# Kernel optimization log

Hardware: AMD Instinct MI355X
Metric: run time of the kernel (lower is better)

Reference implementation:

```python
import jax, jax.numpy as jnp
import numpy as np

KS = 11
SIGMA = 1.5
DATA_RANGE = 1.0
CHANNELS = 3
C1 = (0.01 * DATA_RANGE) ** 2
C2 = (0.03 * DATA_RANGE) ** 2
EPS = 1e-08


def _gaussian_kernel():
    k1d = jnp.linspace(-(KS // 2), KS // 2, KS, dtype=jnp.float32)
    k1d = jnp.exp(-(k1d ** 2) / (2.0 * SIGMA ** 2))
    k2d = jnp.outer(k1d, k1d)
    k2d = k2d / k2d.sum()
    # depthwise kernel: (out_ch=C, in_ch/groups=1, KH, KW)
    return jnp.tile(k2d[None, None], (CHANNELS, 1, 1, 1))


def setup_inputs() -> dict:
    key = jax.random.key(0)
    k1, k2 = jax.random.split(key)
    B, C, H, W = 32, CHANNELS, 512, 512
    pred = jax.random.normal(k1, (B, C, H, W), dtype=jnp.float32)
    target = jax.random.normal(k2, (B, C, H, W), dtype=jnp.float32)
    kernel = _gaussian_kernel()
    return {"pred": pred, "target": target, "kernel": kernel}


def _dwconv(x, kernel):
    pad = KS // 2
    return jax.lax.conv_general_dilated(
        x, kernel,
        window_strides=(1, 1),
        padding=((pad, pad), (pad, pad)),
        dimension_numbers=("NCHW", "OIHW", "NCHW"),
        feature_group_count=CHANNELS,
    )


def reference(pred, target, kernel):
    # map from [-1,1] to [0, data_range]
    p = (pred + 1.0) / 2.0 * DATA_RANGE
    t = (target + 1.0) / 2.0 * DATA_RANGE

    mu_x = _dwconv(p, kernel)
    mu_y = _dwconv(t, kernel)
    sigma_x = _dwconv(p * p, kernel) - mu_x * mu_x
    sigma_y = _dwconv(t * t, kernel) - mu_y * mu_y
    sigma_xy = _dwconv(p * t, kernel) - mu_x * mu_y

    num = (2.0 * mu_x * mu_y + C1) * (2.0 * sigma_xy + C2)
    den = (mu_x ** 2 + mu_y ** 2 + C1) * (sigma_x + sigma_y + C2)
    ssim_map = num / (den + EPS)
    return jnp.mean(ssim_map, axis=(1, 2, 3))  # per-image SSIM, shape (B,)
```

## Files before the change

kernel.cpp:

```cpp
#include <hip/hip_runtime.h>

typedef float v2f __attribute__((ext_vector_type(2)));
typedef float v4f __attribute__((ext_vector_type(4)));

#define KS     11
#define HWDIM  512
#define IMG    (HWDIM*HWDIM)
#define TH     16
#define STRIPS 32
#define PLANES 96
#define EG2    2
#define QW     132
#define NPARTIAL (PLANES*STRIPS)

__device__ __forceinline__ float ssim_px(float mu_u, float mu_v, float Su, float Sv)
{
    const float C1v = 1e-4f, C2v = 9e-4f, EPSV = 1e-8f;
    const float uu = mu_u*mu_u, vv = mu_v*mu_v;
    const float mu2d = 0.5f*(uu - vv);
    const float mu2s = 0.5f*(uu + vv);
    const float Sd   = 0.5f*(Su - Sv);
    const float Ss   = 0.5f*(Su + Sv);
    const float A  = mu2d + C1v;
    const float B  = Sd - mu2d + C2v;
    const float Cc = mu2s + C1v;
    const float D  = Ss - mu2s + C2v;
    return A * B * __builtin_amdgcn_rcpf(Cc*D + EPSV);
}

#define LOADUV(Y, A, B, C, D) do {                                            \
    if ((unsigned)(Y) < HWDIM) {                                              \
        const v4f p4 = *(const v4f*)(pR + (size_t)(Y)*HWDIM);                 \
        const v4f t4 = *(const v4f*)(tR + (size_t)(Y)*HWDIM);                 \
        A = (v2f){0.5f*(p4.x + t4.x) + 1.0f, 0.5f*(p4.x - t4.x)};             \
        B = (v2f){0.5f*(p4.y + t4.y) + 1.0f, 0.5f*(p4.y - t4.y)};             \
        C = (v2f){0.5f*(p4.z + t4.z) + 1.0f, 0.5f*(p4.z - t4.z)};             \
        D = (v2f){0.5f*(p4.w + t4.w) + 1.0f, 0.5f*(p4.w - t4.w)};             \
    } else { A=(v2f)(0.f); B=(v2f)(0.f); C=(v2f)(0.f); D=(v2f)(0.f); }        \
} while(0)

#define VTAP(W, S) do {                                                       \
    v2f t_;                                                                   \
    t_ = (W)*A##S; mA += t_; SA = __builtin_elementwise_fma(t_, A##S, SA);    \
    t_ = (W)*B##S; mB += t_; SB = __builtin_elementwise_fma(t_, B##S, SB);    \
    t_ = (W)*C##S; mC += t_; SC = __builtin_elementwise_fma(t_, C##S, SC);    \
    t_ = (W)*D##S; mD += t_; SD = __builtin_elementwise_fma(t_, D##S, SD);    \
} while(0)

#define HF(ACC, W, T)                                                         \
    ACC = __builtin_elementwise_fma((v4f){(W),(W),(W),(W)}, (T), ACC)

__global__ __launch_bounds__(128) void ssim_stream_kernel(
    const float* __restrict__ pred,
    const float* __restrict__ target,
    const float* __restrict__ kern,
    float* __restrict__ partial)
{
    __shared__ v4f Pq[2][4][QW];
    __shared__ float red[2];

    const int tid   = threadIdx.x;
    const int strip = blockIdx.x;
    const int plane = blockIdx.y;
    const int y0    = strip * TH;

    const float inv_a5 = 1.0f / sqrtf(kern[60]);
    const float w0  = kern[55]*inv_a5,  w1 = kern[56]*inv_a5;
    const float w2  = kern[57]*inv_a5,  w3 = kern[58]*inv_a5;
    const float w4  = kern[59]*inv_a5,  w5 = kern[60]*inv_a5;
    const float w6  = kern[61]*inv_a5,  w7 = kern[62]*inv_a5;
    const float w8  = kern[63]*inv_a5,  w9 = kern[64]*inv_a5;
    const float w10 = kern[65]*inv_a5;

    const float* pR = pred   + (size_t)plane * IMG + 4*tid;
    const float* tR = target + (size_t)plane * IMG + 4*tid;

    if (tid < EG2) {
        const v4f z = (v4f)(0.f);
        #pragma unroll
        for (int par = 0; par < 2; ++par)
            #pragma unroll
            for (int k = 0; k < 4; ++k) {
                Pq[par][k][tid] = z;
                Pq[par][k][EG2 + 128 + tid] = z;
            }
    }

    v2f A0,A1,A2,A3,A4,A5,A6,A7,A8,A9,A10;
    v2f B0,B1,B2,B3,B4,B5,B6,B7,B8,B9,B10;
    v2f C0,C1,C2,C3,C4,C5,C6,C7,C8,C9,C10;
    v2f D0,D1,D2,D3,D4,D5,D6,D7,D8,D9,D10;
    v2f nA, nB, nC, nD;

    A0=(v2f)(0.f); B0=(v2f)(0.f); C0=(v2f)(0.f); D0=(v2f)(0.f);
    LOADUV(y0-5, A1, B1, C1, D1);
    LOADUV(y0-4, A2, B2, C2, D2);
    LOADUV(y0-3, A3, B3, C3, D3);
    LOADUV(y0-2, A4, B4, C4, D4);
    LOADUV(y0-1, A5, B5, C5, D5);
    LOADUV(y0+0, A6, B6, C6, D6);
    LOADUV(y0+1, A7, B7, C7, D7);
    LOADUV(y0+2, A8, B8, C8, D8);
    LOADUV(y0+3, A9, B9, C9, D9);
    LOADUV(y0+4, A10, B10, C10, D10);
    LOADUV(y0+5, nA, nB, nC, nD);

    float lsum = 0.f;
    for (int r = 0; r < TH; ++r) {
        A0=A1; B0=B1; C0=C1; D0=D1;
        A1=A2; B1=B2; C1=C2; D1=D2;
        A2=A3; B2=B3; C2=C3; D2=D3;
        A3=A4; B3=B4; C3=C4; D3=D4;
        A4=A5; B4=B5; C4=C5; D4=D5;
        A5=A6; B5=B6; C5=C6; D5=D6;
        A6=A7; B6=B7; C6=C7; D6=D7;
        A7=A8; B7=B8; C7=C8; D7=D8;
        A8=A9; B8=B9; C8=C9; D8=D9;
        A9=A10; B9=B10; C9=C10; D9=D10;
        A10=nA; B10=nB; C10=nC; D10=nD;
        LOADUV(y0 + r + 6, nA, nB, nC, nD);

        v2f mA=(v2f)(0.f), SA=(v2f)(0.f), mB=(v2f)(0.f), SB=(v2f)(0.f);
        v2f mC=(v2f)(0.f), SC=(v2f)(0.f), mD=(v2f)(0.f), SD=(v2f)(0.f);
        VTAP(w0,0);  VTAP(w1,1);  VTAP(w2,2);  VTAP(w3,3);  VTAP(w4,4);
        VTAP(w5,5);  VTAP(w6,6);  VTAP(w7,7);  VTAP(w8,8);  VTAP(w9,9);
        VTAP(w10,10);

        v4f (*P)[QW] = Pq[r & 1];
        P[0][EG2 + tid] = (v4f){mA.x, mA.y, SA.x, SA.y};
        P[1][EG2 + tid] = (v4f){mB.x, mB.y, SB.x, SB.y};
        P[2][EG2 + tid] = (v4f){mC.x, mC.y, SC.x, SC.y};
        P[3][EG2 + tid] = (v4f){mD.x, mD.y, SD.x, SD.y};
        __syncthreads();

        v4f ac0=(v4f)(0.f), ac1=(v4f)(0.f), ac2=(v4f)(0.f), ac3=(v4f)(0.f);
        {
            v4f q;
            q = P[3][EG2+tid-2]; HF(ac0,w0,q);
            q = P[0][EG2+tid-1]; HF(ac0,w1,q); HF(ac1,w0,q);
            q = P[1][EG2+tid-1]; HF(ac0,w2,q); HF(ac1,w1,q); HF(ac2,w0,q);
            q = P[2][EG2+tid-1]; HF(ac0,w3,q); HF(ac1,w2,q); HF(ac2,w1,q); HF(ac3,w0,q);
            q = P[3][EG2+tid-1]; HF(ac0,w4,q); HF(ac1,w3,q); HF(ac2,w2,q); HF(ac3,w1,q);
            q = P[0][EG2+tid  ]; HF(ac0,w5,q); HF(ac1,w4,q); HF(ac2,w3,q); HF(ac3,w2,q);
            q = P[1][EG2+tid  ]; HF(ac0,w6,q); HF(ac1,w5,q); HF(ac2,w4,q); HF(ac3,w3,q);
            q = P[2][EG2+tid  ]; HF(ac0,w7,q); HF(ac1,w6,q); HF(ac2,w5,q); HF(ac3,w4,q);
            q = P[3][EG2+tid  ]; HF(ac0,w8,q); HF(ac1,w7,q); HF(ac2,w6,q); HF(ac3,w5,q);
            q = P[0][EG2+tid+1]; HF(ac0,w9,q); HF(ac1,w8,q); HF(ac2,w7,q); HF(ac3,w6,q);
            q = P[1][EG2+tid+1]; HF(ac0,w10,q);HF(ac1,w9,q); HF(ac2,w8,q); HF(ac3,w7,q);
            q = P[2][EG2+tid+1];               HF(ac1,w10,q);HF(ac2,w9,q); HF(ac3,w8,q);
            q = P[3][EG2+tid+1];                             HF(ac2,w10,q);HF(ac3,w9,q);
            q = P[0][EG2+tid+2];                                           HF(ac3,w10,q);
        }
        lsum += ssim_px(ac0.x, ac0.y, ac0.z, ac0.w);
        lsum += ssim_px(ac1.x, ac1.y, ac1.z, ac1.w);
        lsum += ssim_px(ac2.x, ac2.y, ac2.z, ac2.w);
        lsum += ssim_px(ac3.x, ac3.y, ac3.z, ac3.w);
    }

    #pragma unroll
    for (int off = 32; off > 0; off >>= 1)
        lsum += __shfl_down(lsum, off, 64);
    if ((tid & 63) == 0) red[tid >> 6] = lsum;
    __syncthreads();
    if (tid == 0)
        partial[plane * STRIPS + strip] = red[0] + red[1];
}

__global__ __launch_bounds__(64) void ssim_reduce_kernel(
    const float* __restrict__ partial,
    float* __restrict__ out)
{
    const int b    = blockIdx.x;
    const int lane = threadIdx.x;
    float s = partial[b * 96 + lane];
    if (lane < 32) s += partial[b * 96 + 64 + lane];
    #pragma unroll
    for (int off = 32; off > 0; off >>= 1)
        s += __shfl_down(s, off, 64);
    if (lane == 0) out[b] = s * (1.0f / (3.0f * 512.0f * 512.0f));
}

extern "C" void kernel_launch(void* const* d_in, const int* in_sizes, int n_in,
                              void* d_out, int out_size, void* d_ws, size_t ws_size,
                              hipStream_t stream) {
    (void)in_sizes; (void)n_in; (void)out_size; (void)ws_size;
    const float* pred   = (const float*)d_in[0];
    const float* target = (const float*)d_in[1];
    const float* kern   = (const float*)d_in[2];
    float* out     = (float*)d_out;
    float* partial = (float*)d_ws;

    dim3 grid(STRIPS, PLANES);
    ssim_stream_kernel<<<grid, 128, 0, stream>>>(pred, target, kern, partial);
    ssim_reduce_kernel<<<32, 64, 0, stream>>>(partial, out);
}
```

Measured before the change: 109.4 us.

## Double strip height and pack two independent strips per 256-thread block

Each strip now covers 32 rows instead of 16, which halves the 10-row vertical halo reloaded per strip. Two strips share one 256-thread block, each with its own shared-memory buffers, and the launch grid is halved to match. The per-row barrier becomes a raw s_barrier preceded by an explicit LDS wait, and the reduce kernel is updated for 48 partials per image. The trade-off is fewer blocks overall (768) and a block-wide barrier that couples two otherwise independent strips.

```diff
diff --git a/kernel.cpp b/kernel.cpp
--- a/kernel.cpp
+++ b/kernel.cpp
@@ -6,8 +6,8 @@
 #define KS     11
 #define HWDIM  512
 #define IMG    (HWDIM*HWDIM)
-#define TH     16
-#define STRIPS 32
+#define TH     32
+#define STRIPS 16
 #define PLANES 96
 #define EG2    2
 #define QW     132
@@ -50,17 +50,19 @@
 #define HF(ACC, W, T)                                                         \
     ACC = __builtin_elementwise_fma((v4f){(W),(W),(W),(W)}, (T), ACC)
 
-__global__ __launch_bounds__(128) void ssim_stream_kernel(
+__global__ __launch_bounds__(256) void ssim_stream_kernel(
     const float* __restrict__ pred,
     const float* __restrict__ target,
     const float* __restrict__ kern,
     float* __restrict__ partial)
 {
-    __shared__ v4f Pq[2][4][QW];
-    __shared__ float red[2];
+    __shared__ v4f Pq[2][2][4][QW];
+    __shared__ float red[4];
 
     const int tid   = threadIdx.x;
-    const int strip = blockIdx.x;
+    const int sub   = tid >> 7;
+    const int st    = tid & 127;
+    const int strip = blockIdx.x * 2 + sub;
     const int plane = blockIdx.y;
     const int y0    = strip * TH;
 
@@ -72,17 +74,17 @@
     const float w8  = kern[63]*inv_a5,  w9 = kern[64]*inv_a5;
     const float w10 = kern[65]*inv_a5;
 
-    const float* pR = pred   + (size_t)plane * IMG + 4*tid;
-    const float* tR = target + (size_t)plane * IMG + 4*tid;
-
-    if (tid < EG2) {
+    const float* pR = pred   + (size_t)plane * IMG + 4*st;
+    const float* tR = target + (size_t)plane * IMG + 4*st;
+
+    if (st < EG2) {
         const v4f z = (v4f)(0.f);
         #pragma unroll
         for (int par = 0; par < 2; ++par)
             #pragma unroll
             for (int k = 0; k < 4; ++k) {
-                Pq[par][k][tid] = z;
-                Pq[par][k][EG2 + 128 + tid] = z;
+                Pq[sub][par][k][st] = z;
+                Pq[sub][par][k][EG2 + 128 + st] = z;
             }
     }
 
@@ -126,30 +128,33 @@
         VTAP(w5,5);  VTAP(w6,6);  VTAP(w7,7);  VTAP(w8,8);  VTAP(w9,9);
         VTAP(w10,10);
 
-        v4f (*P)[QW] = Pq[r & 1];
-        P[0][EG2 + tid] = (v4f){mA.x, mA.y, SA.x, SA.y};
-        P[1][EG2 + tid] = (v4f){mB.x, mB.y, SB.x, SB.y};
-        P[2][EG2 + tid] = (v4f){mC.x, mC.y, SC.x, SC.y};
-        P[3][EG2 + tid] = (v4f){mD.x, mD.y, SD.x, SD.y};
-        __syncthreads();
+        v4f (*P)[QW] = Pq[sub][r & 1];
+        P[0][EG2 + st] = (v4f){mA.x, mA.y, SA.x, SA.y};
+        P[1][EG2 + st] = (v4f){mB.x, mB.y, SB.x, SB.y};
+        P[2][EG2 + st] = (v4f){mC.x, mC.y, SC.x, SC.y};
+        P[3][EG2 + st] = (v4f){mD.x, mD.y, SD.x, SD.y};
+
+        asm volatile("s_waitcnt lgkmcnt(0)" ::: "memory");
+        __builtin_amdgcn_s_barrier();
+        asm volatile("" ::: "memory");
 
         v4f ac0=(v4f)(0.f), ac1=(v4f)(0.f), ac2=(v4f)(0.f), ac3=(v4f)(0.f);
         {
             v4f q;
-            q = P[3][EG2+tid-2]; HF(ac0,w0,q);
-            q = P[0][EG2+tid-1]; HF(ac0,w1,q); HF(ac1,w0,q);
-            q = P[1][EG2+tid-1]; HF(ac0,w2,q); HF(ac1,w1,q); HF(ac2,w0,q);
-            q = P[2][EG2+tid-1]; HF(ac0,w3,q); HF(ac1,w2,q); HF(ac2,w1,q); HF(ac3,w0,q);
-            q = P[3][EG2+tid-1]; HF(ac0,w4,q); HF(ac1,w3,q); HF(ac2,w2,q); HF(ac3,w1,q);
-            q = P[0][EG2+tid  ]; HF(ac0,w5,q); HF(ac1,w4,q); HF(ac2,w3,q); HF(ac3,w2,q);
-            q = P[1][EG2+tid  ]; HF(ac0,w6,q); HF(ac1,w5,q); HF(ac2,w4,q); HF(ac3,w3,q);
-            q = P[2][EG2+tid  ]; HF(ac0,w7,q); HF(ac1,w6,q); HF(ac2,w5,q); HF(ac3,w4,q);
-            q = P[3][EG2+tid  ]; HF(ac0,w8,q); HF(ac1,w7,q); HF(ac2,w6,q); HF(ac3,w5,q);
-            q = P[0][EG2+tid+1]; HF(ac0,w9,q); HF(ac1,w8,q); HF(ac2,w7,q); HF(ac3,w6,q);
-            q = P[1][EG2+tid+1]; HF(ac0,w10,q);HF(ac1,w9,q); HF(ac2,w8,q); HF(ac3,w7,q);
-            q = P[2][EG2+tid+1];               HF(ac1,w10,q);HF(ac2,w9,q); HF(ac3,w8,q);
-            q = P[3][EG2+tid+1];                             HF(ac2,w10,q);HF(ac3,w9,q);
-            q = P[0][EG2+tid+2];                                           HF(ac3,w10,q);
+            q = P[3][EG2+st-2]; HF(ac0,w0,q);
+            q = P[0][EG2+st-1]; HF(ac0,w1,q); HF(ac1,w0,q);
+            q = P[1][EG2+st-1]; HF(ac0,w2,q); HF(ac1,w1,q); HF(ac2,w0,q);
+            q = P[2][EG2+st-1]; HF(ac0,w3,q); HF(ac1,w2,q); HF(ac2,w1,q); HF(ac3,w0,q);
+            q = P[3][EG2+st-1]; HF(ac0,w4,q); HF(ac1,w3,q); HF(ac2,w2,q); HF(ac3,w1,q);
+            q = P[0][EG2+st  ]; HF(ac0,w5,q); HF(ac1,w4,q); HF(ac2,w3,q); HF(ac3,w2,q);
+            q = P[1][EG2+st  ]; HF(ac0,w6,q); HF(ac1,w5,q); HF(ac2,w4,q); HF(ac3,w3,q);
+            q = P[2][EG2+st  ]; HF(ac0,w7,q); HF(ac1,w6,q); HF(ac2,w5,q); HF(ac3,w4,q);
+            q = P[3][EG2+st  ]; HF(ac0,w8,q); HF(ac1,w7,q); HF(ac2,w6,q); HF(ac3,w5,q);
+            q = P[0][EG2+st+1]; HF(ac0,w9,q); HF(ac1,w8,q); HF(ac2,w7,q); HF(ac3,w6,q);
+            q = P[1][EG2+st+1]; HF(ac0,w10,q);HF(ac1,w9,q); HF(ac2,w8,q); HF(ac3,w7,q);
+            q = P[2][EG2+st+1];               HF(ac1,w10,q);HF(ac2,w9,q); HF(ac3,w8,q);
+            q = P[3][EG2+st+1];                             HF(ac2,w10,q);HF(ac3,w9,q);
+            q = P[0][EG2+st+2];                                           HF(ac3,w10,q);
         }
         lsum += ssim_px(ac0.x, ac0.y, ac0.z, ac0.w);
         lsum += ssim_px(ac1.x, ac1.y, ac1.z, ac1.w);
@@ -162,8 +167,8 @@
         lsum += __shfl_down(lsum, off, 64);
     if ((tid & 63) == 0) red[tid >> 6] = lsum;
     __syncthreads();
-    if (tid == 0)
-        partial[plane * STRIPS + strip] = red[0] + red[1];
+    if (st == 0)
+        partial[plane * STRIPS + strip] = red[sub*2] + red[sub*2 + 1];
 }
 
 __global__ __launch_bounds__(64) void ssim_reduce_kernel(
@@ -172,8 +177,7 @@
 {
     const int b    = blockIdx.x;
     const int lane = threadIdx.x;
-    float s = partial[b * 96 + lane];
-    if (lane < 32) s += partial[b * 96 + 64 + lane];
+    float s = (lane < 48) ? partial[b * 48 + lane] : 0.f;
     #pragma unroll
     for (int off = 32; off > 0; off >>= 1)
         s += __shfl_down(s, off, 64);
@@ -190,7 +194,7 @@
     float* out     = (float*)d_out;
     float* partial = (float*)d_ws;
 
-    dim3 grid(STRIPS, PLANES);
-    ssim_stream_kernel<<<grid, 128, 0, stream>>>(pred, target, kern, partial);
+    dim3 grid(STRIPS/2, PLANES);
+    ssim_stream_kernel<<<grid, 256, 0, stream>>>(pred, target, kern, partial);
     ssim_reduce_kernel<<<32, 64, 0, stream>>>(partial, out);
 }
```

Result: faster. 104.1 us (-4.8%).
